# Performance work log

Measured on AMD Instinct MI355X. Metric: run time of the kernel, lower is better.

Reference implementation:

```python
import jax, jax.numpy as jnp
import numpy as np

N = 20000      # nodes
E = 320000     # edges (before self loops)
IN = 16        # input node feature dim
H = 4          # heads (layers 1,2)
C = 128        # per-head channels
HC = H * C     # 512
MLP = 128
NEG_SLOPE = 0.2
EPS = 1e-5


def setup_inputs() -> dict:
    key = jax.random.key(0)
    ks = iter(jax.random.split(key, 64))
    def nrm(shape, scale=0.05):
        return jax.random.normal(next(ks), shape, jnp.float32) * scale
    d = {}
    d["x"] = jax.random.normal(next(ks), (N, IN), jnp.float32)
    d["edge_index"] = jax.random.randint(next(ks), (2, E), 0, N)
    d["edge_weight"] = jax.random.uniform(next(ks), (E, 1), jnp.float32)
    d["node_to_assign_idx"] = 123
    # GATv2 layer 1: in=16 -> 4 heads x 128, concat
    d["Wl1"] = nrm((HC, IN)); d["bl1"] = jnp.zeros((HC,), jnp.float32)
    d["Wr1"] = nrm((HC, IN)); d["br1"] = jnp.zeros((HC,), jnp.float32)
    d["We1"] = nrm((HC, 1)); d["att1"] = nrm((1, H, C)); d["bo1"] = jnp.zeros((HC,), jnp.float32)
    # GATv2 layer 2: in=512 -> 4 heads x 128, concat
    d["Wl2"] = nrm((HC, HC)); d["bl2"] = jnp.zeros((HC,), jnp.float32)
    d["Wr2"] = nrm((HC, HC)); d["br2"] = jnp.zeros((HC,), jnp.float32)
    d["We2"] = nrm((HC, 1)); d["att2"] = nrm((1, H, C)); d["bo2"] = jnp.zeros((HC,), jnp.float32)
    # GATv2 layer 3: in=512 -> 1 head x 128, no concat
    d["Wl3"] = nrm((C, HC)); d["bl3"] = jnp.zeros((C,), jnp.float32)
    d["Wr3"] = nrm((C, HC)); d["br3"] = jnp.zeros((C,), jnp.float32)
    d["We3"] = nrm((C, 1)); d["att3"] = nrm((1, 1, C)); d["bo3"] = jnp.zeros((C,), jnp.float32)
    # LayerNorms
    d["g1"] = jnp.ones((HC,), jnp.float32); d["b1"] = jnp.zeros((HC,), jnp.float32)
    d["g2"] = jnp.ones((HC,), jnp.float32); d["b2"] = jnp.zeros((HC,), jnp.float32)
    d["g3"] = jnp.ones((C,), jnp.float32); d["b3"] = jnp.zeros((C,), jnp.float32)
    # policy / value heads
    d["Pw1"] = nrm((MLP, C)); d["Pb1"] = jnp.zeros((MLP,), jnp.float32)
    d["Pw2"] = nrm((2, MLP)); d["Pb2"] = jnp.zeros((2,), jnp.float32)
    d["Vw1"] = nrm((MLP, C)); d["Vb1"] = jnp.zeros((MLP,), jnp.float32)
    d["Vw2"] = nrm((1, MLP)); d["Vb2"] = jnp.zeros((1,), jnp.float32)
    return d


def layer_norm(x, g, b):
    mu = x.mean(-1, keepdims=True)
    var = ((x - mu) ** 2).mean(-1, keepdims=True)
    return (x - mu) / jnp.sqrt(var + EPS) * g + b


def gatv2(x, src, dst, ea, Wl, bl, Wr, br, We, att, bo, heads, outc, concat):
    """PyG GATv2Conv (eval mode, add_self_loops=True, fill_value='mean')."""
    n = x.shape[0]
    xl = (x @ Wl.T + bl).reshape(n, heads, outc)   # lin_l(x) -> source side
    xr = (x @ Wr.T + br).reshape(n, heads, outc)   # lin_r(x) -> dest side
    e = (ea @ We.T).reshape(-1, heads, outc)       # lin_edge(edge_attr)
    m = xl[src] + xr[dst] + e                      # [Etot, H, C]
    alpha = (jax.nn.leaky_relu(m, NEG_SLOPE) * att).sum(-1)  # [Etot, H]
    amax = jax.ops.segment_max(alpha, dst, num_segments=n)
    alpha = jnp.exp(alpha - amax[dst])
    denom = jax.ops.segment_sum(alpha, dst, num_segments=n)
    alpha = alpha / (denom[dst] + 1e-16)
    out = jax.ops.segment_sum(xl[src] * alpha[..., None], dst, num_segments=n)  # [n, H, C]
    out = out.reshape(n, heads * outc) if concat else out.mean(axis=1)
    return out + bo


def reference(x, edge_index, edge_weight, node_to_assign_idx,
              Wl1, bl1, Wr1, br1, We1, att1, bo1,
              Wl2, bl2, Wr2, br2, We2, att2, bo2,
              Wl3, bl3, Wr3, br3, We3, att3, bo3,
              g1, b1, g2, b2, g3, b3,
              Pw1, Pb1, Pw2, Pb2, Vw1, Vb1, Vw2, Vb2):
    n = x.shape[0]
    loops = jnp.arange(n)
    src = jnp.concatenate([edge_index[0], loops])
    dst = jnp.concatenate([edge_index[1], loops])
    ea_loop = jnp.broadcast_to(edge_weight.mean(0, keepdims=True), (n, edge_weight.shape[1]))
    ea = jnp.concatenate([edge_weight, ea_loop], axis=0)

    h = gatv2(x, src, dst, ea, Wl1, bl1, Wr1, br1, We1, att1, bo1, H, C, True)
    h = jax.nn.elu(layer_norm(h, g1, b1))
    h = gatv2(h, src, dst, ea, Wl2, bl2, Wr2, br2, We2, att2, bo2, H, C, True)
    h = jax.nn.elu(layer_norm(h, g2, b2))
    h = gatv2(h, src, dst, ea, Wl3, bl3, Wr3, br3, We3, att3, bo3, 1, C, False)
    h = layer_norm(h, g3, b3)

    z = h[node_to_assign_idx]                      # [C]
    logits = jax.nn.relu(z @ Pw1.T + Pb1) @ Pw2.T + Pb2   # [2]
    value = jax.nn.relu(z @ Vw1.T + Vb1) @ Vw2.T + Vb2    # [1]
    return (logits, value)
```

## Files before the change

### kernel.cpp

```cpp
#include <hip/hip_runtime.h>
#include <math.h>

#define NEG_SLOPE 0.2f

typedef unsigned short u16;
typedef unsigned int u32;
typedef __attribute__((ext_vector_type(8))) short bf16x8;
typedef __attribute__((ext_vector_type(8))) _Float16 f16x8;
typedef __attribute__((ext_vector_type(2))) _Float16 f16x2;
typedef __attribute__((ext_vector_type(4))) float f32x4;

__device__ __forceinline__ float wave_sum(float v){
  #pragma unroll
  for (int o = 1; o < 64; o <<= 1) v += __shfl_xor(v, o, 64);
  return v;
}

__device__ __forceinline__ u16 f2bf(float f){
  u32 u = __float_as_uint(f);
  return (u16)((u + 0x7FFF + ((u >> 16) & 1)) >> 16);
}
__device__ __forceinline__ float bf2f(u16 h){
  return __uint_as_float(((u32)h) << 16);
}

__device__ __forceinline__ void gl_lds16(const void* g, void* l){
  __builtin_amdgcn_global_load_lds((const __attribute__((address_space(1))) u32*)g,
                                   (__attribute__((address_space(3))) u32*)l, 16, 0, 0);
}

__device__ __forceinline__ float alpha8(f16x8 hv, f16x8 xrh, _Float16 wh, f16x8 weh, f16x8 ath){
  f16x8 tv = hv + xrh + weh*wh;
  f16x8 zero = {0,0,0,0,0,0,0,0};
  f16x8 pos = __builtin_elementwise_max(tv, zero);
  f16x8 neg = __builtin_elementwise_min(tv, zero);
  f16x8 lk  = pos + neg*(_Float16)NEG_SLOPE;
  float p = 0.f;
#if __has_builtin(__builtin_amdgcn_fdot2)
  #pragma unroll
  for (int i = 0; i < 4; i++){
    f16x2 a = {lk[2*i], lk[2*i+1]};
    f16x2 b = {ath[2*i], ath[2*i+1]};
    p = __builtin_amdgcn_fdot2(a, b, p, false);
  }
#else
  #pragma unroll
  for (int j = 0; j < 8; j++) p += (float)lk[j]*(float)ath[j];
#endif
  return p;
}

__global__ void k_prep(const int* __restrict__ dst, const float* __restrict__ ew, int E,
                       int* __restrict__ deg, float* __restrict__ sum_ew){
  float s = 0.f;
  for (int i = blockIdx.x*blockDim.x + threadIdx.x; i < E; i += gridDim.x*blockDim.x){
    atomicAdd(&deg[dst[i]], 1);
    s += ew[i];
  }
  s = wave_sum(s);
  __shared__ float red[4];
  int lane = threadIdx.x & 63, wid = threadIdx.x >> 6;
  if (lane == 0) red[wid] = s;
  __syncthreads();
  if (threadIdx.x == 0){
    float t = 0.f;
    for (int i = 0; i < (int)(blockDim.x >> 6); i++) t += red[i];
    atomicAdd(sum_ew, t);
  }
}

__global__ __launch_bounds__(1024) void k_scan(const int* __restrict__ deg, int* __restrict__ rowptr,
                                               int* __restrict__ cursor, int n){
  __shared__ int sums[1024];
  int t = threadIdx.x;
  int CH = (n + 1023) >> 10;
  int base = t*CH;
  int local = 0;
  for (int i = 0; i < CH; i++){ int idx = base + i; if (idx < n) local += deg[idx] + 1; }
  sums[t] = local;
  __syncthreads();
  for (int off = 1; off < 1024; off <<= 1){
    int v = (t >= off) ? sums[t-off] : 0;
    __syncthreads();
    sums[t] += v;
    __syncthreads();
  }
  int run = sums[t] - local;
  for (int i = 0; i < CH; i++){
    int idx = base + i;
    if (idx < n){ rowptr[idx] = run; cursor[idx] = run; run += deg[idx] + 1; }
  }
  if (t == 0) rowptr[n] = sums[1023];
}

__global__ void k_scatter(const int* __restrict__ ei, const float* __restrict__ ew, int E, int n,
                          const float* __restrict__ sum_ew, int* __restrict__ cursor,
                          int* __restrict__ csr_src, float* __restrict__ csr_w){
  int i = blockIdx.x*blockDim.x + threadIdx.x;
  if (i >= E + n) return;
  if (i < E){
    int s = ei[i];
    int d = ei[E + i];
    int pos = atomicAdd(&cursor[d], 1);
    csr_src[pos] = s; csr_w[pos] = ew[i];
  } else {
    int v = i - E;
    int pos = atomicAdd(&cursor[v], 1);
    csr_src[pos] = v; csr_w[pos] = (*sum_ew) / (float)E;
  }
}

__global__ void k_splitW(const float* __restrict__ Wl2, const float* __restrict__ Wr2,
                         const float* __restrict__ Wl3, const float* __restrict__ Wr3,
                         u16* __restrict__ W2lh, u16* __restrict__ W2rh,
                         u16* __restrict__ W3lh, u16* __restrict__ W3rh){
  int i = blockIdx.x*blockDim.x + threadIdx.x;
  if (i < 262144)      W2lh[i]          = f2bf(Wl2[i]);
  else if (i < 524288) W2rh[i - 262144] = f2bf(Wr2[i - 262144]);
  else if (i < 589824) W3lh[i - 524288] = f2bf(Wl3[i - 524288]);
  else if (i < 655360) W3rh[i - 589824] = f2bf(Wr3[i - 589824]);
}

__global__ __launch_bounds__(256) void k_lin1(const float* __restrict__ x,
        const float* __restrict__ Wl, const float* __restrict__ bl,
        const float* __restrict__ Wr, const float* __restrict__ br,
        _Float16* __restrict__ xl, _Float16* __restrict__ xr, int n){
  __shared__ float Ws[16][1028];
  __shared__ float bs[1024];
  __shared__ float xs[32][16];
  int t = threadIdx.x;
  for (int i = t; i < 512*16; i += 256){
    int j = i >> 4, k = i & 15;
    Ws[k][j] = Wl[i];
    Ws[k][512 + j] = Wr[i];
  }
  for (int i = t; i < 512; i += 256){ bs[i] = bl[i]; bs[512 + i] = br[i]; }
  int n0 = blockIdx.x * 32;
  for (int i = t; i < 32*16; i += 256){ int r = i >> 4, k = i & 15; xs[r][k] = x[(size_t)(n0 + r)*16 + k]; }
  __syncthreads();
  for (int idx = t; idx < 32*1024; idx += 256){
    int r = idx >> 10, c = idx & 1023;
    float s = bs[c];
    #pragma unroll
    for (int k = 0; k < 16; k++) s += xs[r][k] * Ws[k][c];
    int nn = n0 + r;
    if (c < 512) xl[(size_t)nn*512 + c] = (_Float16)s;
    else         xr[(size_t)nn*512 + (c - 512)] = (_Float16)s;
  }
}

__global__ __launch_bounds__(256,4) void k_gemm_mfma(
    const u16* __restrict__ Ah, const u16* __restrict__ Al,
    const u16* __restrict__ Wlh, const u16* __restrict__ Wrh,
    const float* __restrict__ biasl, const float* __restrict__ biasr,
    _Float16* __restrict__ outl, _Float16* __restrict__ outr,
    int n, int K, int J){
  __shared__ __align__(16) u16 lds[12288];
  u16* lA_h = lds;
  u16* lA_l = lds + 4096;
  u16* lW   = lds + 8192;
  int t = threadIdx.x;
  int lane = t & 63, w = t >> 6;
  int lane15 = lane & 15, lgrp = lane >> 4;
  int jb = J >> 7;
  int side = blockIdx.x / jb;
  int j0 = (blockIdx.x - side*jb) * 128;
  const u16* Wh = side ? Wrh : Wlh;
  const float* bias = side ? biasr : biasl;
  _Float16* out = side ? outr : outl;
  int n0 = blockIdx.y * 128;
  int wm = (w >> 1) * 64, wn = (w & 1) * 64;
  f32x4 acc[4][4] = {};

  int s0 = t, s1 = t + 256;
  int r0 = s0 >> 2, r1 = s1 >> 2;
  int sl0 = (s0 & 3) ^ ((r0 >> 1) & 3);
  int sl1 = (s1 & 3) ^ ((r1 >> 1) & 3);
  size_t arow0 = (size_t)min(n0 + r0, n - 1) * K + sl0*8;
  size_t arow1 = (size_t)min(n0 + r1, n - 1) * K + sl1*8;
  size_t wrow0 = (size_t)(j0 + r0) * K + sl0*8;
  size_t wrow1 = (size_t)(j0 + r1) * K + sl1*8;

  int rcol = (lgrp * 16) ^ (((lane15 >> 1) & 3) << 4);

  for (int k0 = 0; k0 < K; k0 += 32){
    gl_lds16(Ah + arow0 + k0, lA_h + s0*8);
    gl_lds16(Ah + arow1 + k0, lA_h + s1*8);
    gl_lds16(Al + arow0 + k0, lA_l + s0*8);
    gl_lds16(Al + arow1 + k0, lA_l + s1*8);
    gl_lds16(Wh + wrow0 + k0, lW + s0*8);
    gl_lds16(Wh + wrow1 + k0, lW + s1*8);
    __syncthreads();
    bf16x8 ah[4], al[4], bh[4];
    #pragma unroll
    for (int i = 0; i < 4; i++){
      int qa = (wm + i*16 + lane15)*64 + rcol;
      ah[i]  = *(const bf16x8*)((const char*)lA_h + qa);
      al[i]  = *(const bf16x8*)((const char*)lA_l + qa);
      int qb = (wn + i*16 + lane15)*64 + rcol;
      bh[i]  = *(const bf16x8*)((const char*)lW + qb);
    }
    #pragma unroll
    for (int mi = 0; mi < 4; mi++)
      #pragma unroll
      for (int ni = 0; ni < 4; ni++){
        acc[mi][ni] = __builtin_amdgcn_mfma_f32_16x16x32_bf16(al[mi], bh[ni], acc[mi][ni], 0, 0, 0);
        acc[mi][ni] = __builtin_amdgcn_mfma_f32_16x16x32_bf16(ah[mi], bh[ni], acc[mi][ni], 0, 0, 0);
      }
    __syncthreads();
  }

  #pragma unroll
  for (int ni = 0; ni < 4; ni++){
    int col = j0 + wn + ni*16 + lane15;
    float bia = bias[col];
    #pragma unroll
    for (int mi = 0; mi < 4; mi++){
      int rowb = n0 + wm + mi*16 + lgrp*4;
      #pragma unroll
      for (int rg = 0; rg < 4; rg++){
        int row = rowb + rg;
        if (row < n) out[(size_t)row*J + col] = (_Float16)(acc[mi][ni][rg] + bia);
      }
    }
  }
}

__global__ __launch_bounds__(256) void k_agg4(
                      const _Float16* __restrict__ xl, const _Float16* __restrict__ xr,
                      const float* __restrict__ We, const float* __restrict__ att, const float* __restrict__ bo,
                      const float* __restrict__ gam, const float* __restrict__ bet,
                      const int* __restrict__ rowptr, const int* __restrict__ csr_src,
                      const float* __restrict__ csr_w,
                      u16* __restrict__ oh, u16* __restrict__ ol, int n){
  constexpr int HC_ = 512;
  constexpr float RT = 8.f;
  constexpr int NB = 4;
  int t = threadIdx.x, lane = t & 63, w = t >> 6;
  int l16 = lane & 15, grp = lane >> 4;
  int c0 = w*128 + l16*8;

  float4 wea = *(const float4*)&We[c0],  web = *(const float4*)&We[c0 + 4];
  float4 ata = *(const float4*)&att[c0], atb = *(const float4*)&att[c0 + 4];
  float4 boa = *(const float4*)&bo[c0],  bob = *(const float4*)&bo[c0 + 4];
  float4 ga  = *(const float4*)&gam[c0], gb  = *(const float4*)&gam[c0 + 4];
  float4 ba  = *(const float4*)&bet[c0], bb  = *(const float4*)&bet[c0 + 4];
  float we8[8] = {wea.x,wea.y,wea.z,wea.w,web.x,web.y,web.z,web.w};
  float at8[8] = {ata.x,ata.y,ata.z,ata.w,atb.x,atb.y,atb.z,atb.w};
  float bo8[8] = {boa.x,boa.y,boa.z,boa.w,bob.x,bob.y,bob.z,bob.w};
  float g8[8]  = {ga.x,ga.y,ga.z,ga.w,gb.x,gb.y,gb.z,gb.w};
  float b8[8]  = {ba.x,ba.y,ba.z,ba.w,bb.x,bb.y,bb.z,bb.w};
  f16x8 weh, ath;
  #pragma unroll
  for (int j = 0; j < 8; j++){ weh[j] = (_Float16)we8[j]; ath[j] = (_Float16)at8[j]; }

  __shared__ float red[4][2];

  #pragma unroll 1
  for (int ib = 0; ib < NB; ib++){
    int nid = blockIdx.x*NB + ib;
    if (nid >= n) break;

    f16x8 xrh = *(const f16x8*)(xr + (size_t)nid*HC_ + c0);

    int rs = rowptr[nid], re = rowptr[nid + 1];
    float m = -3e38f, d = 0.f;
    float acc[8] = {};
    for (int e0 = rs + grp; e0 < re; e0 += 8){
      int e1 = e0 + 4;
      bool has1 = e1 < re;
      int s0 = csr_src[e0];
      int s1 = has1 ? csr_src[e1] : s0;
      float w0 = csr_w[e0];
      float w1 = has1 ? csr_w[e1] : 0.f;
      f16x8 hv0 = *(const f16x8*)(xl + (size_t)s0*HC_ + c0);
      f16x8 hv1 = *(const f16x8*)(xl + (size_t)s1*HC_ + c0);
      float p0 = alpha8(hv0, xrh, (_Float16)w0, weh, ath);
      float p1 = alpha8(hv1, xrh, (_Float16)w1, weh, ath);
      #pragma unroll
      for (int o = 1; o < 16; o <<= 1){
        p0 += __shfl_xor(p0, o, 64);
        p1 += __shfl_xor(p1, o, 64);
      }
      if (!has1) p1 = -3e38f;
      float pm = fmaxf(p0, p1);
      if (pm > m + RT){
        float sc = __expf(m - pm);
        d *= sc;
        #pragma unroll
        for (int j = 0; j < 8; j++) acc[j] *= sc;
        m = pm;
      }
      float e0x = __expf(p0 - m), e1x = __expf(p1 - m);
      d += e0x + e1x;
      float v0[8], v1[8];
      #pragma unroll
      for (int j = 0; j < 8; j++){ v0[j] = (float)hv0[j]; v1[j] = (float)hv1[j]; }
      #pragma unroll
      for (int j = 0; j < 8; j++) acc[j] += e0x*v0[j] + e1x*v1[j];
    }
    float M = m;
    M = fmaxf(M, __shfl_xor(M, 16, 64));
    M = fmaxf(M, __shfl_xor(M, 32, 64));
    float sc = __expf(m - M);
    float dd = d * sc;
    dd += __shfl_xor(dd, 16, 64);
    dd += __shfl_xor(dd, 32, 64);
    #pragma unroll
    for (int j = 0; j < 8; j++){
      float a = acc[j] * sc;
      a += __shfl_xor(a, 16, 64);
      a += __shfl_xor(a, 32, 64);
      acc[j] = a;
    }
    float inv = 1.f / (dd + 1e-16f);
    float o8[8];
    #pragma unroll
    for (int j = 0; j < 8; j++) o8[j] = acc[j]*inv + bo8[j];

    float s1 = 0.f, s2 = 0.f;
    #pragma unroll
    for (int j = 0; j < 8; j++){ s1 += o8[j]; s2 += o8[j]*o8[j]; }
    #pragma unroll
    for (int o = 1; o < 16; o <<= 1){ s1 += __shfl_xor(s1, o, 64); s2 += __shfl_xor(s2, o, 64); }
    __syncthreads();
    if (lane == 0){ red[w][0] = s1; red[w][1] = s2; }
    __syncthreads();
    float S1 = red[0][0] + red[1][0] + red[2][0] + red[3][0];
    float S2 = red[0][1] + red[1][1] + red[2][1] + red[3][1];
    float mu = S1 / (float)HC_;
    float var = S2 / (float)HC_ - mu*mu;
    float rstd = rsqrtf(var + 1e-5f);
    float y[8];
    #pragma unroll
    for (int j = 0; j < 8; j++){
      float yy = (o8[j] - mu)*rstd*g8[j] + b8[j];
      y[j] = (yy > 0.f) ? yy : (__expf(yy) - 1.f);
    }
    if (grp == 0){
      u32 hv2[4], lv2[4];
      #pragma unroll
      for (int j = 0; j < 4; j++){
        u16 h0 = f2bf(y[2*j]), h1 = f2bf(y[2*j+1]);
        u16 l0 = f2bf(y[2*j] - bf2f(h0)), l1 = f2bf(y[2*j+1] - bf2f(h1));
        hv2[j] = (u32)h0 | ((u32)h1 << 16);
        lv2[j] = (u32)l0 | ((u32)l1 << 16);
      }
      *(uint4*)&oh[(size_t)nid*HC_ + c0] = make_uint4(hv2[0],hv2[1],hv2[2],hv2[3]);
      *(uint4*)&ol[(size_t)nid*HC_ + c0] = make_uint4(lv2[0],lv2[1],lv2[2],lv2[3]);
    }
  }
}

__global__ __launch_bounds__(64) void k_agg1(
                      const _Float16* __restrict__ xl, const _Float16* __restrict__ xr,
                      const float* __restrict__ We, const float* __restrict__ att, const float* __restrict__ bo,
                      const float* __restrict__ gam, const float* __restrict__ bet,
                      const int* __restrict__ rowptr, const int* __restrict__ csr_src,
                      const float* __restrict__ csr_w,
                      float* __restrict__ out, int n){
  constexpr float RT = 8.f;
  int lane = threadIdx.x;
  int l16 = lane & 15, grp = lane >> 4;
  int c0 = l16*8;

  float4 wea = *(const float4*)&We[c0],  web = *(const float4*)&We[c0 + 4];
  float4 ata = *(const float4*)&att[c0], atb = *(const float4*)&att[c0 + 4];
  float4 boa = *(const float4*)&bo[c0],  bob = *(const float4*)&bo[c0 + 4];
  float4 ga  = *(const float4*)&gam[c0], gb  = *(const float4*)&gam[c0 + 4];
  float4 ba  = *(const float4*)&bet[c0], bb  = *(const float4*)&bet[c0 + 4];
  float we8[8] = {wea.x,wea.y,wea.z,wea.w,web.x,web.y,web.z,web.w};
  float at8[8] = {ata.x,ata.y,ata.z,ata.w,atb.x,atb.y,atb.z,atb.w};
  float bo8[8] = {boa.x,boa.y,boa.z,boa.w,bob.x,bob.y,bob.z,bob.w};
  float g8[8]  = {ga.x,ga.y,ga.z,ga.w,gb.x,gb.y,gb.z,gb.w};
  float b8[8]  = {ba.x,ba.y,ba.z,ba.w,bb.x,bb.y,bb.z,bb.w};
  f16x8 weh, ath;
  #pragma unroll
  for (int j = 0; j < 8; j++){ weh[j] = (_Float16)we8[j]; ath[j] = (_Float16)at8[j]; }

  int nid = blockIdx.x*4 + grp;
  if (nid >= n) return;

  f16x8 xrh = *(const f16x8*)(xr + (size_t)nid*128 + c0);
  int rs = rowptr[nid], re = rowptr[nid + 1];
  float m = -3e38f, d = 0.f;
  float acc[8] = {};
  for (int e0 = rs; e0 < re; e0 += 2){
    int e1 = e0 + 1;
    bool has1 = e1 < re;
    int s0 = csr_src[e0];
    int s1 = has1 ? csr_src[e1] : s0;
    float w0 = csr_w[e0];
    float w1 = has1 ? csr_w[e1] : 0.f;
    f16x8 hv0 = *(const f16x8*)(xl + (size_t)s0*128 + c0);
    f16x8 hv1 = *(const f16x8*)(xl + (size_t)s1*128 + c0);
    float p0 = alpha8(hv0, xrh, (_Float16)w0, weh, ath);
    float p1 = alpha8(hv1, xrh, (_Float16)w1, weh, ath);
    #pragma unroll
    for (int o = 1; o < 16; o <<= 1){
      p0 += __shfl_xor(p0, o, 64);
      p1 += __shfl_xor(p1, o, 64);
    }
    if (!has1) p1 = -3e38f;
    float pm = fmaxf(p0, p1);
    if (pm > m + RT){
      float sc = __expf(m - pm);
      d *= sc;
      #pragma unroll
      for (int j = 0; j < 8; j++) acc[j] *= sc;
      m = pm;
    }
    float e0x = __expf(p0 - m), e1x = __expf(p1 - m);
    d += e0x + e1x;
    float v0[8], v1[8];
    #pragma unroll
    for (int j = 0; j < 8; j++){ v0[j] = (float)hv0[j]; v1[j] = (float)hv1[j]; }
    #pragma unroll
    for (int j = 0; j < 8; j++) acc[j] += e0x*v0[j] + e1x*v1[j];
  }
  float inv = 1.f / (d + 1e-16f);
  float o8[8];
  #pragma unroll
  for (int j = 0; j < 8; j++) o8[j] = acc[j]*inv + bo8[j];

  float s1 = 0.f, s2 = 0.f;
  #pragma unroll
  for (int j = 0; j < 8; j++){ s1 += o8[j]; s2 += o8[j]*o8[j]; }
  #pragma unroll
  for (int o = 1; o < 16; o <<= 1){ s1 += __shfl_xor(s1, o, 64); s2 += __shfl_xor(s2, o, 64); }
  float mu = s1 / 128.f;
  float var = s2 / 128.f - mu*mu;
  float rstd = rsqrtf(var + 1e-5f);
  float y[8];
  #pragma unroll
  for (int j = 0; j < 8; j++) y[j] = (o8[j] - mu)*rstd*g8[j] + b8[j];
  float* orow = out + (size_t)nid*128 + c0;
  *(float4*)orow       = make_float4(y[0],y[1],y[2],y[3]);
  *(float4*)(orow + 4) = make_float4(y[4],y[5],y[6],y[7]);
}

__global__ __launch_bounds__(128) void k_heads(const float* __restrict__ h3, const int* __restrict__ idxp,
        const float* __restrict__ Pw1, const float* __restrict__ Pb1,
        const float* __restrict__ Pw2, const float* __restrict__ Pb2,
        const float* __restrict__ Vw1, const float* __restrict__ Vb1,
        const float* __restrict__ Vw2, const float* __restrict__ Vb2,
        float* __restrict__ out){
  __shared__ float z[128], hp[128], hv[128];
  int t = threadIdx.x;
  int idx = *idxp;
  z[t] = h3[(size_t)idx*128 + t];
  __syncthreads();
  float sp = Pb1[t], sv = Vb1[t];
  for (int c = 0; c < 128; c++){
    float zc = z[c];
    sp += Pw1[t*128 + c] * zc;
    sv += Vw1[t*128 + c] * zc;
  }
  hp[t] = fmaxf(sp, 0.f);
  hv[t] = fmaxf(sv, 0.f);
  __syncthreads();
  if (t < 64){
    float l0 = Pw2[t]*hp[t]       + Pw2[64 + t]*hp[64 + t];
    float l1 = Pw2[128 + t]*hp[t] + Pw2[192 + t]*hp[64 + t];
    float vv = Vw2[t]*hv[t]       + Vw2[64 + t]*hv[64 + t];
    #pragma unroll
    for (int o = 1; o < 64; o <<= 1){
      l0 += __shfl_xor(l0, o, 64); l1 += __shfl_xor(l1, o, 64); vv += __shfl_xor(vv, o, 64);
    }
    if (t == 0){ out[0] = l0 + Pb2[0]; out[1] = l1 + Pb2[1]; out[2] = vv + Vb2[0]; }
  }
}

extern "C" void kernel_launch(void* const* d_in, const int* in_sizes, int n_in,
                              void* d_out, int out_size, void* d_ws, size_t ws_size,
                              hipStream_t stream){
  const float* x    = (const float*)d_in[0];
  const int*   ei   = (const int*)d_in[1];
  const float* ew   = (const float*)d_in[2];
  const int*   nidx = (const int*)d_in[3];
  const float* Wl1 = (const float*)d_in[4];  const float* bl1 = (const float*)d_in[5];
  const float* Wr1 = (const float*)d_in[6];  const float* br1 = (const float*)d_in[7];
  const float* We1 = (const float*)d_in[8];  const float* att1 = (const float*)d_in[9];
  const float* bo1 = (const float*)d_in[10];
  const float* Wl2 = (const float*)d_in[11]; const float* bl2 = (const float*)d_in[12];
  const float* Wr2 = (const float*)d_in[13]; const float* br2 = (const float*)d_in[14];
  const float* We2 = (const float*)d_in[15]; const float* att2 = (const float*)d_in[16];
  const float* bo2 = (const float*)d_in[17];
  const float* Wl3 = (const float*)d_in[18]; const float* bl3 = (const float*)d_in[19];
  const float* Wr3 = (const float*)d_in[20]; const float* br3 = (const float*)d_in[21];
  const float* We3 = (const float*)d_in[22]; const float* att3 = (const float*)d_in[23];
  const float* bo3 = (const float*)d_in[24];
  const float* gn1 = (const float*)d_in[25]; const float* bn1 = (const float*)d_in[26];
  const float* gn2 = (const float*)d_in[27]; const float* bn2 = (const float*)d_in[28];
  const float* gn3 = (const float*)d_in[29]; const float* bn3 = (const float*)d_in[30];
  const float* Pw1 = (const float*)d_in[31]; const float* Pb1 = (const float*)d_in[32];
  const float* Pw2 = (const float*)d_in[33]; const float* Pb2 = (const float*)d_in[34];
  const float* Vw1 = (const float*)d_in[35]; const float* Vb1 = (const float*)d_in[36];
  const float* Vw2 = (const float*)d_in[37]; const float* Vb2 = (const float*)d_in[38];

  const int N = in_sizes[0] / 16;
  const int E = in_sizes[2];
  const int NE = N + E;

  char* w = (char*)d_ws;
  size_t off = 0;
  float* sum_ew = (float*)(w + off); off += 256;
  int* rowptr = (int*)(w + off); off += (size_t)(N + 1)*4; off = (off + 255) & ~(size_t)255;
  int* cursor = (int*)(w + off); off += (size_t)N*4;       off = (off + 255) & ~(size_t)255;
  int* deg    = (int*)(w + off); off += (size_t)N*4;       off = (off + 255) & ~(size_t)255;
  int* csr_src= (int*)(w + off); off += (size_t)NE*4;      off = (off + 255) & ~(size_t)255;
  float* csr_w= (float*)(w + off); off += (size_t)NE*4;    off = (off + 255) & ~(size_t)255;
  u16* W2lh = (u16*)(w + off); off += (size_t)512*512*2;
  u16* W2rh = (u16*)(w + off); off += (size_t)512*512*2;
  u16* W3lh = (u16*)(w + off); off += (size_t)128*512*2;
  u16* W3rh = (u16*)(w + off); off += (size_t)128*512*2;
  off = (off + 1048575) & ~(size_t)1048575;
  _Float16* A  = (_Float16*)(w + off); off += (size_t)N*512*2;
  _Float16* B  = (_Float16*)(w + off); off += (size_t)N*512*2;
  u16*   Ch = (u16*)(w + off);   off += (size_t)N*512*2;
  u16*   Cl = (u16*)(w + off);   off += (size_t)N*512*2;
  float* D  = (float*)(w + off); off += (size_t)N*128*4;
  (void)ws_size; (void)n_in; (void)out_size;

  hipMemsetAsync(sum_ew, 0, 4, stream);
  hipMemsetAsync(deg, 0, (size_t)N*4, stream);

  k_prep<<<256, 256, 0, stream>>>(ei + E, ew, E, deg, sum_ew);
  k_scan<<<1, 1024, 0, stream>>>(deg, rowptr, cursor, N);
  k_scatter<<<(NE + 255)/256, 256, 0, stream>>>(ei, ew, E, N, sum_ew, cursor, csr_src, csr_w);
  k_splitW<<<2560, 256, 0, stream>>>(Wl2, Wr2, Wl3, Wr3, W2lh, W2rh, W3lh, W3rh);

  const int GY = (N + 127)/128;

  k_lin1<<<N/32, 256, 0, stream>>>(x, Wl1, bl1, Wr1, br1, A, B, N);
  k_agg4<<<(N + 3)/4, 256, 0, stream>>>(A, B, We1, att1, bo1, gn1, bn1,
                                        rowptr, csr_src, csr_w, Ch, Cl, N);
  k_gemm_mfma<<<dim3(8, GY), 256, 0, stream>>>(Ch, Cl, W2lh, W2rh, bl2, br2, A, B, N, 512, 512);
  k_agg4<<<(N + 3)/4, 256, 0, stream>>>(A, B, We2, att2, bo2, gn2, bn2,
                                        rowptr, csr_src, csr_w, Ch, Cl, N);
  k_gemm_mfma<<<dim3(2, GY), 256, 0, stream>>>(Ch, Cl, W3lh, W3rh, bl3, br3, A, B, N, 512, 128);
  k_agg1<<<(N + 3)/4, 64, 0, stream>>>(A, B, We3, att3, bo3, gn3, bn3,
                                       rowptr, csr_src, csr_w, D, N);
  k_heads<<<1, 128, 0, stream>>>(D, nidx, Pw1, Pb1, Pw2, Pb2, Vw1, Vb1, Vw2, Vb2, (float*)d_out);
}
```

Baseline: 639.5 us.

## Map each agg4 node to a single wave, removing cross-wave LDS reduction

```diff
diff --git a/kernel.cpp b/kernel.cpp
--- a/kernel.cpp
+++ b/kernel.cpp
@@ -226,7 +226,7 @@
   }
 }
 
-__global__ __launch_bounds__(256) void k_agg4(
+__global__ __launch_bounds__(128) void k_agg4(
                       const _Float16* __restrict__ xl, const _Float16* __restrict__ xr,
                       const float* __restrict__ We, const float* __restrict__ att, const float* __restrict__ bo,
                       const float* __restrict__ gam, const float* __restrict__ bet,
@@ -235,39 +235,34 @@
                       u16* __restrict__ oh, u16* __restrict__ ol, int n){
   constexpr int HC_ = 512;
   constexpr float RT = 8.f;
-  constexpr int NB = 4;
-  int t = threadIdx.x, lane = t & 63, w = t >> 6;
+  constexpr int NB = 2;
+  int t = threadIdx.x;
+  int widx = t >> 6, lane = t & 63;
   int l16 = lane & 15, grp = lane >> 4;
-  int c0 = w*128 + l16*8;
+  int c0 = grp*128 + l16*8;
 
   float4 wea = *(const float4*)&We[c0],  web = *(const float4*)&We[c0 + 4];
   float4 ata = *(const float4*)&att[c0], atb = *(const float4*)&att[c0 + 4];
-  float4 boa = *(const float4*)&bo[c0],  bob = *(const float4*)&bo[c0 + 4];
-  float4 ga  = *(const float4*)&gam[c0], gb  = *(const float4*)&gam[c0 + 4];
-  float4 ba  = *(const float4*)&bet[c0], bb  = *(const float4*)&bet[c0 + 4];
-  float we8[8] = {wea.x,wea.y,wea.z,wea.w,web.x,web.y,web.z,web.w};
-  float at8[8] = {ata.x,ata.y,ata.z,ata.w,atb.x,atb.y,atb.z,atb.w};
-  float bo8[8] = {boa.x,boa.y,boa.z,boa.w,bob.x,bob.y,bob.z,bob.w};
-  float g8[8]  = {ga.x,ga.y,ga.z,ga.w,gb.x,gb.y,gb.z,gb.w};
-  float b8[8]  = {ba.x,ba.y,ba.z,ba.w,bb.x,bb.y,bb.z,bb.w};
   f16x8 weh, ath;
   #pragma unroll
-  for (int j = 0; j < 8; j++){ weh[j] = (_Float16)we8[j]; ath[j] = (_Float16)at8[j]; }
-
-  __shared__ float red[4][2];
+  for (int j = 0; j < 4; j++){
+    weh[j] = (_Float16)((&wea.x)[j]); weh[4+j] = (_Float16)((&web.x)[j]);
+    ath[j] = (_Float16)((&ata.x)[j]); ath[4+j] = (_Float16)((&atb.x)[j]);
+  }
 
   #pragma unroll 1
   for (int ib = 0; ib < NB; ib++){
-    int nid = blockIdx.x*NB + ib;
-    if (nid >= n) break;
+    int nid = blockIdx.x*(2*NB) + widx*NB + ib;
+    if (nid >= n) continue;
 
     f16x8 xrh = *(const f16x8*)(xr + (size_t)nid*HC_ + c0);
-
-    int rs = rowptr[nid], re = rowptr[nid + 1];
+    int rs = __builtin_amdgcn_readfirstlane(rowptr[nid]);
+    int re = __builtin_amdgcn_readfirstlane(rowptr[nid + 1]);
+
     float m = -3e38f, d = 0.f;
     float acc[8] = {};
-    for (int e0 = rs + grp; e0 < re; e0 += 8){
-      int e1 = e0 + 4;
+    for (int e0 = rs; e0 < re; e0 += 2){
+      int e1 = e0 + 1;
       bool has1 = e1 < re;
       int s0 = csr_src[e0];
       int s1 = has1 ? csr_src[e1] : s0;
@@ -299,56 +294,43 @@
       #pragma unroll
       for (int j = 0; j < 8; j++) acc[j] += e0x*v0[j] + e1x*v1[j];
     }
-    float M = m;
-    M = fmaxf(M, __shfl_xor(M, 16, 64));
-    M = fmaxf(M, __shfl_xor(M, 32, 64));
-    float sc = __expf(m - M);
-    float dd = d * sc;
-    dd += __shfl_xor(dd, 16, 64);
-    dd += __shfl_xor(dd, 32, 64);
-    #pragma unroll
-    for (int j = 0; j < 8; j++){
-      float a = acc[j] * sc;
-      a += __shfl_xor(a, 16, 64);
-      a += __shfl_xor(a, 32, 64);
-      acc[j] = a;
-    }
-    float inv = 1.f / (dd + 1e-16f);
+    float inv = 1.f / (d + 1e-16f);
+    float4 boa = *(const float4*)&bo[c0], bob = *(const float4*)&bo[c0 + 4];
     float o8[8];
     #pragma unroll
-    for (int j = 0; j < 8; j++) o8[j] = acc[j]*inv + bo8[j];
+    for (int j = 0; j < 4; j++){
+      o8[j]   = acc[j]*inv   + (&boa.x)[j];
+      o8[4+j] = acc[4+j]*inv + (&bob.x)[j];
+    }
 
     float s1 = 0.f, s2 = 0.f;
     #pragma unroll
     for (int j = 0; j < 8; j++){ s1 += o8[j]; s2 += o8[j]*o8[j]; }
     #pragma unroll
-    for (int o = 1; o < 16; o <<= 1){ s1 += __shfl_xor(s1, o, 64); s2 += __shfl_xor(s2, o, 64); }
-    __syncthreads();
-    if (lane == 0){ red[w][0] = s1; red[w][1] = s2; }
-    __syncthreads();
-    float S1 = red[0][0] + red[1][0] + red[2][0] + red[3][0];
-    float S2 = red[0][1] + red[1][1] + red[2][1] + red[3][1];
-    float mu = S1 / (float)HC_;
-    float var = S2 / (float)HC_ - mu*mu;
+    for (int o = 1; o < 64; o <<= 1){ s1 += __shfl_xor(s1, o, 64); s2 += __shfl_xor(s2, o, 64); }
+    float mu = s1 / (float)HC_;
+    float var = s2 / (float)HC_ - mu*mu;
     float rstd = rsqrtf(var + 1e-5f);
+    float4 ga = *(const float4*)&gam[c0], gb = *(const float4*)&gam[c0 + 4];
+    float4 ba = *(const float4*)&bet[c0], bb = *(const float4*)&bet[c0 + 4];
     float y[8];
     #pragma unroll
-    for (int j = 0; j < 8; j++){
-      float yy = (o8[j] - mu)*rstd*g8[j] + b8[j];
-      y[j] = (yy > 0.f) ? yy : (__expf(yy) - 1.f);
-    }
-    if (grp == 0){
-      u32 hv2[4], lv2[4];
-      #pragma unroll
-      for (int j = 0; j < 4; j++){
-        u16 h0 = f2bf(y[2*j]), h1 = f2bf(y[2*j+1]);
-        u16 l0 = f2bf(y[2*j] - bf2f(h0)), l1 = f2bf(y[2*j+1] - bf2f(h1));
-        hv2[j] = (u32)h0 | ((u32)h1 << 16);
-        lv2[j] = (u32)l0 | ((u32)l1 << 16);
-      }
-      *(uint4*)&oh[(size_t)nid*HC_ + c0] = make_uint4(hv2[0],hv2[1],hv2[2],hv2[3]);
-      *(uint4*)&ol[(size_t)nid*HC_ + c0] = make_uint4(lv2[0],lv2[1],lv2[2],lv2[3]);
-    }
+    for (int j = 0; j < 4; j++){
+      float ya = (o8[j]   - mu)*rstd*(&ga.x)[j] + (&ba.x)[j];
+      float yb = (o8[4+j] - mu)*rstd*(&gb.x)[j] + (&bb.x)[j];
+      y[j]   = (ya > 0.f) ? ya : (__expf(ya) - 1.f);
+      y[4+j] = (yb > 0.f) ? yb : (__expf(yb) - 1.f);
+    }
+    u32 hv2[4], lv2[4];
+    #pragma unroll
+    for (int j = 0; j < 4; j++){
+      u16 h0 = f2bf(y[2*j]), h1 = f2bf(y[2*j+1]);
+      u16 l0 = f2bf(y[2*j] - bf2f(h0)), l1 = f2bf(y[2*j+1] - bf2f(h1));
+      hv2[j] = (u32)h0 | ((u32)h1 << 16);
+      lv2[j] = (u32)l0 | ((u32)l1 << 16);
+    }
+    *(uint4*)&oh[(size_t)nid*HC_ + c0] = make_uint4(hv2[0],hv2[1],hv2[2],hv2[3]);
+    *(uint4*)&ol[(size_t)nid*HC_ + c0] = make_uint4(lv2[0],lv2[1],lv2[2],lv2[3]);
   }
 }
 
@@ -369,14 +351,15 @@
   float4 boa = *(const float4*)&bo[c0],  bob = *(const float4*)&bo[c0 + 4];
   float4 ga  = *(const float4*)&gam[c0], gb  = *(const float4*)&gam[c0 + 4];
   float4 ba  = *(const float4*)&bet[c0], bb  = *(const float4*)&bet[c0 + 4];
-  float we8[8] = {wea.x,wea.y,wea.z,wea.w,web.x,web.y,web.z,web.w};
-  float at8[8] = {ata.x,ata.y,ata.z,ata.w,atb.x,atb.y,atb.z,atb.w};
   float bo8[8] = {boa.x,boa.y,boa.z,boa.w,bob.x,bob.y,bob.z,bob.w};
   float g8[8]  = {ga.x,ga.y,ga.z,ga.w,gb.x,gb.y,gb.z,gb.w};
   float b8[8]  = {ba.x,ba.y,ba.z,ba.w,bb.x,bb.y,bb.z,bb.w};
   f16x8 weh, ath;
   #pragma unroll
-  for (int j = 0; j < 8; j++){ weh[j] = (_Float16)we8[j]; ath[j] = (_Float16)at8[j]; }
+  for (int j = 0; j < 4; j++){
+    weh[j] = (_Float16)((&wea.x)[j]); weh[4+j] = (_Float16)((&web.x)[j]);
+    ath[j] = (_Float16)((&ata.x)[j]); ath[4+j] = (_Float16)((&atb.x)[j]);
+  }
 
   int nid = blockIdx.x*4 + grp;
   if (nid >= n) return;
@@ -533,10 +516,10 @@
   const int GY = (N + 127)/128;
 
   k_lin1<<<N/32, 256, 0, stream>>>(x, Wl1, bl1, Wr1, br1, A, B, N);
-  k_agg4<<<(N + 3)/4, 256, 0, stream>>>(A, B, We1, att1, bo1, gn1, bn1,
+  k_agg4<<<(N + 3)/4, 128, 0, stream>>>(A, B, We1, att1, bo1, gn1, bn1,
                                         rowptr, csr_src, csr_w, Ch, Cl, N);
   k_gemm_mfma<<<dim3(8, GY), 256, 0, stream>>>(Ch, Cl, W2lh, W2rh, bl2, br2, A, B, N, 512, 512);
-  k_agg4<<<(N + 3)/4, 256, 0, stream>>>(A, B, We2, att2, bo2, gn2, bn2,
+  k_agg4<<<(N + 3)/4, 128, 0, stream>>>(A, B, We2, att2, bo2, gn2, bn2,
                                         rowptr, csr_src, csr_w, Ch, Cl, N);
   k_gemm_mfma<<<dim3(2, GY), 256, 0, stream>>>(Ch, Cl, W3lh, W3rh, bl3, br3, A, B, N, 512, 128);
   k_agg1<<<(N + 3)/4, 64, 0, stream>>>(A, B, We3, att3, bo3, gn3, bn3,
```

Measured after the change: 535.8 us. 1.19x faster.
